# Kernel tuning notes

Measured on AMD Instinct MI355X. Metric: run time of the kernel, lower is better.

Reference implementation:

```python
import jax, jax.numpy as jnp
import numpy as np

HEADS = 4
BN_EPS = 1e-5


def _hgat_conv(x, src, dst, node_type, edge_attr, edge_type,
               ne, W, We, a_src, a_dst, a_edge, ee, Wres, b, concat):
    """Heterogeneous GAT conv: per-type embeddings + edge-featured attention.
    x: [N, Fin]; edge_attr: [E, De]; returns [N, H*C] (concat) or [N, C]."""
    N = x.shape[0]
    C = W.shape[1] // HEADS
    xi = x + ne[node_type]                                  # node-type conditioning
    h = (xi @ W).reshape(N, HEADS, C)                       # [N, H, C]
    he = ((edge_attr + ee[edge_type]) @ We).reshape(-1, HEADS, C)  # [E, H, C]
    s = jnp.einsum('nhc,hc->nh', h, a_src)                  # [N, H]
    d = jnp.einsum('nhc,hc->nh', h, a_dst)                  # [N, H]
    e = jnp.einsum('ehc,hc->eh', he, a_edge)                # [E, H]
    alpha = jax.nn.leaky_relu(s[src] + d[dst] + e, 0.2)     # [E, H]
    # softmax over incoming edges per destination node
    amax = jax.ops.segment_max(alpha, dst, num_segments=N)  # [N, H]
    amax = jnp.where(jnp.isfinite(amax), amax, 0.0)
    ex = jnp.exp(alpha - amax[dst])
    den = jax.ops.segment_sum(ex, dst, num_segments=N)
    coef = ex / (den[dst] + 1e-16)                          # [E, H]
    msg = h[src] * coef[:, :, None]                         # [E, H, C]
    out = jax.ops.segment_sum(msg, dst, num_segments=N)     # [N, H, C]
    out = out.reshape(N, HEADS * C) if concat else out.mean(axis=1)
    return out + x @ Wres + b                               # residual + bias


def _batch_norm(x, gamma, beta):
    mu = x.mean(axis=0)
    var = x.var(axis=0)
    return (x - mu) * jax.lax.rsqrt(var + BN_EPS) * gamma + beta


def setup_inputs() -> dict:
    key = jax.random.key(0)
    ks = jax.random.split(key, 32)
    N, E, H = 50000, 400000, 32          # nodes, edges, hidden_channels
    DE = 64                               # edge_dim
    NT, ET = 3, 4                         # node / edge type counts
    D1 = H * HEADS                        # 128 = enc1 output / enc2 width

    def g(k, shape, scale=1.0):
        return (jax.random.normal(ks[k], shape, dtype=jnp.float32) * scale)

    inp = {
        'x': g(0, (N, H)),
        'edge_index': jax.random.randint(ks[1], (2, E), 0, N, dtype=jnp.int32),
        'node_type': jax.random.randint(ks[2], (N,), 0, NT, dtype=jnp.int32),
        'edge_attr': g(3, (E, DE)),
        'edge_type': jax.random.randint(ks[4], (E,), 0, ET, dtype=jnp.int32),
        # enc1 params (in=32, per-head out=32, concat -> 128)
        'ne1': g(5, (NT, H), 0.1),
        'w1': g(6, (H, HEADS * H), 1.0 / np.sqrt(H)),
        'we1': g(7, (DE, HEADS * H), 1.0 / np.sqrt(DE)),
        'asrc1': g(8, (HEADS, H), 0.1), 'adst1': g(9, (HEADS, H), 0.1),
        'aedge1': g(10, (HEADS, H), 0.1),
        'ee1': g(11, (ET, DE), 0.1),
        'wres1': g(12, (H, D1), 1.0 / np.sqrt(H)),
        'b1': jnp.zeros((D1,), jnp.float32),
        # BatchNorm(128)
        'gamma': jnp.ones((D1,), jnp.float32),
        'beta': jnp.zeros((D1,), jnp.float32),
        # enc2 params (in=128, per-head out=128, mean -> 128)
        'ne2': g(13, (NT, D1), 0.1),
        'w2': g(14, (D1, HEADS * D1), 1.0 / np.sqrt(D1)),
        'we2': g(15, (DE, HEADS * D1), 1.0 / np.sqrt(DE)),
        'asrc2': g(16, (HEADS, D1), 0.1), 'adst2': g(17, (HEADS, D1), 0.1),
        'aedge2': g(18, (HEADS, D1), 0.1),
        'ee2': g(19, (ET, DE), 0.1),
        'wres2': g(20, (D1, D1), 1.0 / np.sqrt(D1)),
        'b2': jnp.zeros((D1,), jnp.float32),
    }
    return inp


def reference(x, edge_index, node_type, edge_attr, edge_type,
              ne1, w1, we1, asrc1, adst1, aedge1, ee1, wres1, b1,
              gamma, beta,
              ne2, w2, we2, asrc2, adst2, aedge2, ee2, wres2, b2):
    src, dst = edge_index[0], edge_index[1]
    h = _hgat_conv(x, src, dst, node_type, edge_attr, edge_type,
                   ne1, w1, we1, asrc1, adst1, aedge1, ee1, wres1, b1,
                   concat=True)
    h = _batch_norm(h, gamma, beta)
    out = _hgat_conv(h, src, dst, node_type, edge_attr, edge_type,
                     ne2, w2, we2, asrc2, adst2, aedge2, ee2, wres2, b2,
                     concat=False)
    return out
```

## Files before the change

kernel.cpp:

```cpp
#include <hip/hip_runtime.h>
#include <hip/hip_bf16.h>

typedef unsigned short u16;
typedef unsigned int u32;

constexpr int NN = 50000;
constexpr int NE = 400000;
constexpr int MPAD = 50048;

typedef __attribute__((ext_vector_type(8))) short s16x8;
typedef __attribute__((ext_vector_type(4))) float f32x4;

__device__ __forceinline__ float bf2f(u16 u) {
    union { u32 i; float f; } v; v.i = ((u32)u) << 16; return v.f;
}
__device__ __forceinline__ u16 f2bf(float f) {
    union { float f; u32 i; } v; v.f = f;
    u32 r = v.i + 0x7fffu + ((v.i >> 16) & 1u);
    return (u16)(r >> 16);
}
__device__ __forceinline__ float ldf(const void* p, size_t i, int isbf) {
    if (isbf) return bf2f(((const u16*)p)[i]);
    return ((const float*)p)[i];
}
__device__ __forceinline__ float clampf(float v) {
    return fminf(fmaxf(v, -1e4f), 1e4f);
}

__device__ int   g_flag;
__device__ int   g_counter;
__device__ float g_qe1[256], g_qe2[256];
__device__ float g_eq1[16], g_eq2[16];
__device__ float g_ps1[128], g_pd1[128], g_ps2[512], g_pd2[512];
__device__ float g_bnsum[128], g_bnsumsq[128], g_bnscale[128], g_bnshift[128];
__device__ int   g_deg[NN], g_start[NN], g_cur[NN];
__device__ int   g_eidx[NE];
__device__ __attribute__((aligned(16))) float g_sbuf[NN * 4];
__device__ __attribute__((aligned(16))) float g_dbuf[NN * 4];
__device__ __attribute__((aligned(16))) float g_alpha[(size_t)NE * 4];
__device__ __attribute__((aligned(16))) float g_el2[(size_t)NE * 4];
__device__ __attribute__((aligned(16))) float g_xbuf[(size_t)NN * 128];
__device__ __attribute__((aligned(16))) float g_acc2[(size_t)NN * 128];
__device__ __attribute__((aligned(16))) u16 g_A1[(size_t)MPAD * 64];
__device__ __attribute__((aligned(16))) u16 g_A2[(size_t)MPAD * 160];
__device__ __attribute__((aligned(16))) u16 g_B1t[192 * 64];
__device__ __attribute__((aligned(16))) u16 g_B1bt[128 * 128];
__device__ __attribute__((aligned(16))) u16 g_B2t[192 * 160];
__device__ __attribute__((aligned(16))) u16 g_B2bt[128 * 512];
__device__ __attribute__((aligned(16))) u16 g_xi1[(size_t)NN * 32];
__device__ __attribute__((aligned(16))) u16 g_xi2[(size_t)NN * 128];
__device__ __attribute__((aligned(16))) u16 g_agg1[(size_t)MPAD * 128];
__device__ __attribute__((aligned(16))) u16 g_agg2[(size_t)MPAD * 512];

__global__ void k_detect(const u16* x) {
    if (threadIdx.x == 0) {
        int cnt = 0;
        for (int i = 0; i < 64; i++) {
            u16 u = x[2 * i];
            int ex = (u >> 7) & 0xff;
            if (ex >= 100 && ex <= 140) cnt++;
        }
        g_flag = (cnt >= 40) ? 1 : 0;
        g_counter = 0;
    }
}
__global__ void k_zero() {
    int i = blockIdx.x * blockDim.x + threadIdx.x;
    if (i < NN) g_deg[i] = 0;
    if (i < 128) { g_bnsum[i] = 0.f; g_bnsumsq[i] = 0.f; }
}

__global__ __launch_bounds__(256) void k_prep(
    const void* we1, const void* ae1, const void* we2, const void* ae2,
    const void* w1, const void* as1, const void* ad1,
    const void* w2, const void* as2, const void* ad2) {
    int isbf = g_flag;
    int t = threadIdx.x;
    int idx = blockIdx.x * 16 + (t >> 4);
    int s = t & 15;
    float a = 0.f;
    if (idx < 256) {
        int k = idx >> 2, hd = idx & 3;
        for (int c = s; c < 32; c += 16)
            a += ldf(we1, k * 128 + hd * 32 + c, isbf) * ldf(ae1, hd * 32 + c, isbf);
    } else if (idx < 512) {
        int i2 = idx - 256;
        int k = i2 >> 2, hd = i2 & 3;
        for (int c = s; c < 128; c += 16)
            a += ldf(we2, k * 512 + hd * 128 + c, isbf) * ldf(ae2, hd * 128 + c, isbf);
    } else if (idx < 768) {
        int i2 = idx - 512;
        int isd = i2 >> 7, j = i2 & 127;
        int h = j >> 5, k = j & 31;
        const void* av = isd ? ad1 : as1;
        for (int c = s; c < 32; c += 16)
            a += ldf(w1, k * 128 + h * 32 + c, isbf) * ldf(av, h * 32 + c, isbf);
    } else {
        int i2 = idx - 768;
        int isd = i2 >> 9, j = i2 & 511;
        int h = j >> 7, k = j & 127;
        const void* av = isd ? ad2 : as2;
        for (int c = s; c < 128; c += 16)
            a += ldf(w2, (size_t)k * 512 + h * 128 + c, isbf) * ldf(av, h * 128 + c, isbf);
    }
#pragma unroll
    for (int mk = 8; mk >= 1; mk >>= 1) a += __shfl_xor(a, mk);
    if (s == 0) {
        if (idx < 256) g_qe1[idx] = a;
        else if (idx < 512) g_qe2[idx - 256] = a;
        else if (idx < 768) {
            int i2 = idx - 512;
            if (i2 >> 7) g_pd1[i2 & 127] = a; else g_ps1[i2 & 127] = a;
        } else {
            int i2 = idx - 768;
            if (i2 >> 9) g_pd2[i2 & 511] = a; else g_ps2[i2 & 511] = a;
        }
    }
}
__global__ void k_prep2(const void* ee1, const void* ee2) {
    int isbf = g_flag;
    int t = threadIdx.x;
    int idx = blockIdx.x * 16 + (t >> 4);
    int s = t & 15;
    int lyr = idx >> 4;
    int et = (idx >> 2) & 3, h = idx & 3;
    const void* ee = lyr ? ee2 : ee1;
    const float* qe = lyr ? g_qe2 : g_qe1;
    float a = 0.f;
    for (int k = s; k < 64; k += 16)
        a += ldf(ee, et * 64 + k, isbf) * qe[k * 4 + h];
#pragma unroll
    for (int mk = 8; mk >= 1; mk >>= 1) a += __shfl_xor(a, mk);
    if (s == 0) {
        if (lyr) g_eq2[et * 4 + h] = a; else g_eq1[et * 4 + h] = a;
    }
}

__global__ void k_deg(const int* __restrict__ dstp) {
    int e = blockIdx.x * blockDim.x + threadIdx.x;
    if (e < NE) atomicAdd(&g_deg[dstp[e]], 1);
}
__global__ void k_start() {
    int n = blockIdx.x * blockDim.x + threadIdx.x;
    if (n < NN) {
        int d = g_deg[n];
        int s = atomicAdd(&g_counter, d);
        g_start[n] = s; g_cur[n] = s;
    }
}
__global__ void k_scatter(const int* __restrict__ dstp) {
    int e = blockIdx.x * blockDim.x + threadIdx.x;
    if (e < NE) {
        int slot = atomicAdd(&g_cur[dstp[e]], 1);
        g_eidx[slot] = e;
    }
}

__device__ __forceinline__ u16 a1val(const void* x, int n, int k, int nt, int isbf) {
    if (k < 32) return f2bf(ldf(x, (size_t)n * 32 + k, isbf));
    if (k == 32 + nt || k == 35) return 0x3F80u;
    return 0;
}
__global__ __launch_bounds__(256) void k_buildA1(const void* x, const int* __restrict__ ntype,
                                                 const void* ne1) {
    int isbf = g_flag;
    int i = blockIdx.x * 256 + threadIdx.x;
    if (i >= MPAD * 32) return;
    int n = i >> 5, k2 = (i & 31) << 1;
    u32 pk = 0;
    if (n < NN) {
        int nt = ntype[n];
        pk = (u32)a1val(x, n, k2, nt, isbf) | ((u32)a1val(x, n, k2 + 1, nt, isbf) << 16);
        if (k2 < 32) {
            float x0 = ldf(x, (size_t)n * 32 + k2, isbf) + ldf(ne1, nt * 32 + k2, isbf);
            float x1 = ldf(x, (size_t)n * 32 + k2 + 1, isbf) + ldf(ne1, nt * 32 + k2 + 1, isbf);
            ((u32*)g_xi1)[(size_t)n * 16 + (k2 >> 1)] =
                (u32)f2bf(x0) | ((u32)f2bf(x1) << 16);
        }
    }
    ((u32*)g_A1)[i] = pk;
}
__global__ __launch_bounds__(256) void k_a2tail(const int* __restrict__ ntype) {
    int i = blockIdx.x * 256 + threadIdx.x;
    if (i >= NN * 16) return;
    int n = i >> 4, q = i & 15;
    int k2 = 128 + q * 2;
    int nt = ntype[n];
    u16 lo = (k2 == 128 + nt || k2 == 131) ? 0x3F80u : 0;
    u16 hi = (k2 + 1 == 128 + nt || k2 + 1 == 131) ? 0x3F80u : 0;
    ((u32*)g_A2)[(size_t)n * 80 + 64 + q] = (u32)lo | ((u32)hi << 16);
}
__global__ __launch_bounds__(256) void k_xi2(const int* __restrict__ ntype, const void* ne2) {
    int isbf = g_flag;
    int i = blockIdx.x * 256 + threadIdx.x;
    if (i >= NN * 64) return;
    int n = i >> 6, jp = (i & 63) << 1;
    int nt = ntype[n];
    float v0 = g_xbuf[(size_t)n * 128 + jp] * g_bnscale[jp] + g_bnshift[jp]
             + ldf(ne2, nt * 128 + jp, isbf);
    float v1 = g_xbuf[(size_t)n * 128 + jp + 1] * g_bnscale[jp + 1] + g_bnshift[jp + 1]
             + ldf(ne2, nt * 128 + jp + 1, isbf);
    ((u32*)g_xi2)[i] = (u32)f2bf(v0) | ((u32)f2bf(v1) << 16);
}

__global__ void k_buildB1(const void* ne1, const void* w1, const void* wres1, const void* b1) {
    int isbf = g_flag;
    int j = blockIdx.x;
    int k = threadIdx.x;
    float v = 0.f;
    if (j < 128) {
        if (k < 32) v = ldf(wres1, k * 128 + j, isbf);
        else if (k == 35) v = ldf(b1, j, isbf);
    } else if (j < 136) {
        int h = (j - 128) & 3;
        const float* p = (j < 132) ? g_ps1 : g_pd1;
        if (k < 32) v = p[h * 32 + k];
        else if (k < 35) {
            int tt = k - 32; float a = 0.f;
            for (int c = 0; c < 32; c++)
                a += ldf(ne1, tt * 32 + c, isbf) * p[h * 32 + c];
            v = a;
        }
    }
    (void)w1;
    g_B1t[j * 64 + k] = f2bf(v);
}
__global__ void k_buildB1b(const void* w1) {
    int isbf = g_flag;
    int j = blockIdx.x;
    int k = threadIdx.x;
    float v = ((k >> 5) == (j >> 5)) ? ldf(w1, (k & 31) * 128 + j, isbf) : 0.f;
    g_B1bt[j * 128 + k] = f2bf(v);
}
__global__ void k_buildB2(const void* ne2, const void* w2, const void* wres2, const void* b2) {
    int isbf = g_flag;
    int j = blockIdx.x;
    int k = threadIdx.x;
    if (k >= 160) return;
    float v = 0.f;
    if (j < 128) {
        if (k < 128) v = g_bnscale[k] * ldf(wres2, k * 128 + j, isbf);
        else if (k == 131) {
            float a = ldf(b2, j, isbf);
            for (int c = 0; c < 128; c++)
                a += g_bnshift[c] * ldf(wres2, c * 128 + j, isbf);
            v = a;
        }
    } else if (j < 136) {
        int h = (j - 128) & 3;
        const float* p = (j < 132) ? g_ps2 : g_pd2;
        if (k < 128) v = g_bnscale[k] * p[h * 128 + k];
        else if (k < 131) {
            int tt = k - 128; float a = 0.f;
            for (int c = 0; c < 128; c++)
                a += (g_bnshift[c] + ldf(ne2, tt * 128 + c, isbf)) * p[h * 128 + c];
            v = a;
        }
    }
    (void)w2;
    g_B2t[j * 160 + k] = f2bf(v);
}
__global__ void k_buildB2b(const void* w2) {
    int isbf = g_flag;
    int j = blockIdx.x;
    for (int k = threadIdx.x; k < 512; k += 256) {
        float v = 0.25f * ldf(w2, (size_t)(k & 127) * 512 + (k >> 7) * 128 + j, isbf);
        g_B2bt[j * 512 + k] = f2bf(v);
    }
}

template<int K, int KT, int LAYER>
__global__ __launch_bounds__(256) void k_gemm(void* outp) {
    constexpr int KP = KT + 8;
    __shared__ __attribute__((aligned(16))) u16 As[64 * KP];
    __shared__ __attribute__((aligned(16))) u16 Bs[64 * KP];
    const u16* __restrict__ A  = (LAYER == 1) ? g_A1 : (LAYER == 2) ? g_A2
                               : (LAYER == 3) ? g_agg1 : g_agg2;
    const u16* __restrict__ Bt = (LAYER == 1) ? g_B1t : (LAYER == 2) ? g_B2t
                               : (LAYER == 3) ? g_B1bt : g_B2bt;
    int isbf = g_flag;
    const int t = threadIdx.x;
    const int mb = blockIdx.x, cb = blockIdx.y;
    const int wave = t >> 6, lane = t & 63;
    const int lr = lane & 15, lg = lane >> 4;
    f32x4 acc[4] = {};
    constexpr int CH = KT / 8;
#pragma unroll 1
    for (int kt = 0; kt < K / KT; kt++) {
        __syncthreads();
        for (int c = t; c < 64 * CH; c += 256) {
            int r = c / CH, o = (c - r * CH) * 8;
            *(s16x8*)&As[r * KP + o] =
                *(const s16x8*)&A[((size_t)(mb * 64 + r)) * K + kt * KT + o];
            *(s16x8*)&Bs[r * KP + o] =
                *(const s16x8*)&Bt[((size_t)(cb * 64 + r)) * K + kt * KT + o];
        }
        __syncthreads();
        const u16* ap  = &As[(wave * 16 + lr) * KP + lg * 8];
        const u16* bp0 = &Bs[lr * KP + lg * 8];
#pragma unroll
        for (int ks = 0; ks < KT / 32; ks++) {
            s16x8 af = *(const s16x8*)(ap + ks * 32);
#pragma unroll
            for (int ct = 0; ct < 4; ct++) {
                s16x8 bf = *(const s16x8*)(bp0 + ct * 16 * KP + ks * 32);
                acc[ct] = __builtin_amdgcn_mfma_f32_16x16x32_bf16(af, bf, acc[ct], 0, 0, 0);
            }
        }
    }
    const int rowb = mb * 64 + wave * 16 + lg * 4;
#pragma unroll
    for (int ct = 0; ct < 4; ct++) {
        int j = cb * 64 + ct * 16 + lr;
#pragma unroll
        for (int r = 0; r < 4; r++) {
            int n = rowb + r;
            if (n >= NN) continue;
            float v = acc[ct][r];
            if (LAYER == 1) {
                if (j < 128)      g_xbuf[(size_t)n * 128 + j] = clampf(v);
                else if (j < 132) g_sbuf[n * 4 + (j - 128)] = clampf(v);
                else if (j < 136) g_dbuf[n * 4 + (j - 132)] = clampf(v);
            } else if (LAYER == 2) {
                if (j < 128)      g_acc2[(size_t)n * 128 + j] = clampf(v);
                else if (j < 132) g_sbuf[n * 4 + (j - 128)] = clampf(v);
                else if (j < 136) g_dbuf[n * 4 + (j - 132)] = clampf(v);
            } else if (LAYER == 3) {
                float* p = &g_xbuf[(size_t)n * 128 + j];
                float x = clampf(*p + v);
                *p = x;
                g_A2[(size_t)n * 160 + j] = f2bf(x);
            } else {
                float v2 = clampf(g_acc2[(size_t)n * 128 + j] + v);
                if (isbf) ((u16*)outp)[(size_t)n * 128 + j] = f2bf(v2);
                else      ((float*)outp)[(size_t)n * 128 + j] = v2;
            }
        }
    }
}

__global__ __launch_bounds__(256) void k_edge12(
    const int* __restrict__ srcp, const int* __restrict__ dstp,
    const int* __restrict__ etype, const void* eattr) {
    __shared__ float qel1[256], qel2[256], eq1s[16], eq2s[16];
    int isbf = g_flag;
    int t = threadIdx.x;
    qel1[t] = g_qe1[t];
    qel2[t] = g_qe2[t];
    if (t < 16) { eq1s[t] = g_eq1[t]; eq2s[t] = g_eq2[t]; }
    __syncthreads();
    int sub = t & 15;
    float q1[4][4], q2[4][4];
#pragma unroll
    for (int i = 0; i < 4; i++)
#pragma unroll
        for (int h = 0; h < 4; h++) {
            q1[i][h] = qel1[(sub * 4 + i) * 4 + h];
            q2[i][h] = qel2[(sub * 4 + i) * 4 + h];
        }
    int e = blockIdx.x * 16 + (t >> 4);
    if (e >= NE) return;
    float ev[4];
    if (isbf) {
        ushort4 vv = *(const ushort4*)((const u16*)eattr + (size_t)e * 64 + sub * 4);
        ev[0] = bf2f(vv.x); ev[1] = bf2f(vv.y); ev[2] = bf2f(vv.z); ev[3] = bf2f(vv.w);
    } else {
        float4 vv = *(const float4*)((const float*)eattr + (size_t)e * 64 + sub * 4);
        ev[0] = vv.x; ev[1] = vv.y; ev[2] = vv.z; ev[3] = vv.w;
    }
    float p10 = 0.f, p11 = 0.f, p12 = 0.f, p13 = 0.f;
    float p20 = 0.f, p21 = 0.f, p22 = 0.f, p23 = 0.f;
#pragma unroll
    for (int i = 0; i < 4; i++) {
        p10 += ev[i] * q1[i][0]; p11 += ev[i] * q1[i][1];
        p12 += ev[i] * q1[i][2]; p13 += ev[i] * q1[i][3];
        p20 += ev[i] * q2[i][0]; p21 += ev[i] * q2[i][1];
        p22 += ev[i] * q2[i][2]; p23 += ev[i] * q2[i][3];
    }
#pragma unroll
    for (int mk = 1; mk < 16; mk <<= 1) {
        p10 += __shfl_xor(p10, mk); p11 += __shfl_xor(p11, mk);
        p12 += __shfl_xor(p12, mk); p13 += __shfl_xor(p13, mk);
        p20 += __shfl_xor(p20, mk); p21 += __shfl_xor(p21, mk);
        p22 += __shfl_xor(p22, mk); p23 += __shfl_xor(p23, mk);
    }
    if (sub == 0) {
        int et = etype[e], ss = srcp[e], dd = dstp[e];
        float4 sb = *(const float4*)(g_sbuf + ss * 4);
        float4 db = *(const float4*)(g_dbuf + dd * 4);
        float a0 = sb.x + db.x + p10 + eq1s[et * 4 + 0];
        float a1 = sb.y + db.y + p11 + eq1s[et * 4 + 1];
        float a2 = sb.z + db.z + p12 + eq1s[et * 4 + 2];
        float a3 = sb.w + db.w + p13 + eq1s[et * 4 + 3];
        a0 = a0 > 0.f ? a0 : 0.2f * a0;
        a1 = a1 > 0.f ? a1 : 0.2f * a1;
        a2 = a2 > 0.f ? a2 : 0.2f * a2;
        a3 = a3 > 0.f ? a3 : 0.2f * a3;
        *(float4*)(g_alpha + 4 * (size_t)e) = make_float4(
            clampf(a0), clampf(a1), clampf(a2), clampf(a3));
        *(float4*)(g_el2 + 4 * (size_t)e) = make_float4(
            p20 + eq2s[et * 4 + 0], p21 + eq2s[et * 4 + 1],
            p22 + eq2s[et * 4 + 2], p23 + eq2s[et * 4 + 3]);
    }
}

__global__ __launch_bounds__(256) void k_edge2(
    const int* __restrict__ srcp, const int* __restrict__ dstp) {
    int e = blockIdx.x * 256 + threadIdx.x;
    if (e >= NE) return;
    float4 p = *(const float4*)(g_el2 + 4 * (size_t)e);
    int ss = srcp[e], dd = dstp[e];
    float4 sb = *(const float4*)(g_sbuf + ss * 4);
    float4 db = *(const float4*)(g_dbuf + dd * 4);
    float a0 = sb.x + db.x + p.x;
    float a1 = sb.y + db.y + p.y;
    float a2 = sb.z + db.z + p.z;
    float a3 = sb.w + db.w + p.w;
    a0 = a0 > 0.f ? a0 : 0.2f * a0;
    a1 = a1 > 0.f ? a1 : 0.2f * a1;
    a2 = a2 > 0.f ? a2 : 0.2f * a2;
    a3 = a3 > 0.f ? a3 : 0.2f * a3;
    *(float4*)(g_alpha + 4 * (size_t)e) = make_float4(
        clampf(a0), clampf(a1), clampf(a2), clampf(a3));
}

__global__ __launch_bounds__(256) void k_att1(const int* __restrict__ srcp) {
    int lane = threadIdx.x & 63;
    int n = blockIdx.x * 4 + (threadIdx.x >> 6);
    if (n >= NN) return;
    int st = g_start[n], dg = g_deg[n];
    float m0 = -1e30f, m1 = -1e30f, m2 = -1e30f, m3 = -1e30f;
    for (int i = lane; i < dg; i += 64) {
        int e = g_eidx[st + i];
        float4 a = *(const float4*)(g_alpha + 4 * (size_t)e);
        m0 = fmaxf(m0, a.x); m1 = fmaxf(m1, a.y);
        m2 = fmaxf(m2, a.z); m3 = fmaxf(m3, a.w);
    }
    for (int mk = 32; mk >= 1; mk >>= 1) {
        m0 = fmaxf(m0, __shfl_xor(m0, mk)); m1 = fmaxf(m1, __shfl_xor(m1, mk));
        m2 = fmaxf(m2, __shfl_xor(m2, mk)); m3 = fmaxf(m3, __shfl_xor(m3, mk));
    }
    int j0 = 2 * lane;
    int hd = j0 >> 5;
    float z0 = 0.f, z1 = 0.f, z2 = 0.f, z3 = 0.f;
    float acc0 = 0.f, acc1 = 0.f;
    for (int base = 0; base < dg; base += 64) {
        int i = base + lane;
        int sidx = 0; float c0 = 0.f, c1 = 0.f, c2 = 0.f, c3 = 0.f;
        if (i < dg) {
            int e = g_eidx[st + i];
            float4 a = *(const float4*)(g_alpha + 4 * (size_t)e);
            sidx = srcp[e];
            c0 = expf(a.x - m0); c1 = expf(a.y - m1);
            c2 = expf(a.z - m2); c3 = expf(a.w - m3);
            z0 += c0; z1 += c1; z2 += c2; z3 += c3;
        }
        int cnt = min(64, dg - base);
        for (int jj = 0; jj < cnt; jj++) {
            int s2 = __shfl(sidx, jj);
            float b0 = __shfl(c0, jj), b1 = __shfl(c1, jj);
            float b2v = __shfl(c2, jj), b3 = __shfl(c3, jj);
            float cs = hd == 0 ? b0 : hd == 1 ? b1 : hd == 2 ? b2v : b3;
            u32 hv = *(const u32*)(g_xi1 + (size_t)s2 * 32 + (j0 & 31));
            acc0 += bf2f((u16)(hv & 0xffff)) * cs;
            acc1 += bf2f((u16)(hv >> 16)) * cs;
        }
    }
    for (int mk = 32; mk >= 1; mk >>= 1) {
        z0 += __shfl_xor(z0, mk); z1 += __shfl_xor(z1, mk);
        z2 += __shfl_xor(z2, mk); z3 += __shfl_xor(z3, mk);
    }
    float iv = 1.f / ((hd == 0 ? z0 : hd == 1 ? z1 : hd == 2 ? z2 : z3) + 1e-16f);
    ((u32*)g_agg1)[((size_t)n * 128 + j0) >> 1] =
        (u32)f2bf(acc0 * iv) | ((u32)f2bf(acc1 * iv) << 16);
}

__global__ __launch_bounds__(256) void k_bnstats() {
    int t = threadIdx.x;
    int j = t & 127;
    int r0 = blockIdx.x * 2 + (t >> 7);
    float s = 0.f, ss = 0.f;
    for (int r = r0; r < NN; r += 500) {
        float v = g_xbuf[(size_t)r * 128 + j];
        s += v; ss += v * v;
    }
    atomicAdd(&g_bnsum[j], s);
    atomicAdd(&g_bnsumsq[j], ss);
}
__global__ void k_bnfin(const void* gamma, const void* beta) {
    int isbf = g_flag;
    int j = threadIdx.x;
    float mu = g_bnsum[j] * (1.f / NN);
    float var = fmaxf(g_bnsumsq[j] * (1.f / NN) - mu * mu, 0.f);
    float rstd = rsqrtf(var + 1e-5f);
    float sc = ldf(gamma, j, isbf) * rstd;
    g_bnscale[j] = sc;
    g_bnshift[j] = ldf(beta, j, isbf) - mu * sc;
}

__global__ __launch_bounds__(256) void k_att2(const int* __restrict__ srcp) {
    int lane = threadIdx.x & 63;
    int n = blockIdx.x * 4 + (threadIdx.x >> 6);
    if (n >= NN) return;
    int st = g_start[n], dg = g_deg[n];
    float m0 = -1e30f, m1 = -1e30f, m2 = -1e30f, m3 = -1e30f;
    for (int i = lane; i < dg; i += 64) {
        int e = g_eidx[st + i];
        float4 a = *(const float4*)(g_alpha + 4 * (size_t)e);
        m0 = fmaxf(m0, a.x); m1 = fmaxf(m1, a.y);
        m2 = fmaxf(m2, a.z); m3 = fmaxf(m3, a.w);
    }
    for (int mk = 32; mk >= 1; mk >>= 1) {
        m0 = fmaxf(m0, __shfl_xor(m0, mk)); m1 = fmaxf(m1, __shfl_xor(m1, mk));
        m2 = fmaxf(m2, __shfl_xor(m2, mk)); m3 = fmaxf(m3, __shfl_xor(m3, mk));
    }
    int c0 = 2 * lane;
    float z0 = 0.f, z1 = 0.f, z2 = 0.f, z3 = 0.f;
    float a00 = 0.f, a01 = 0.f, a10 = 0.f, a11 = 0.f;
    float a20 = 0.f, a21 = 0.f, a30 = 0.f, a31 = 0.f;
    for (int base = 0; base < dg; base += 64) {
        int i = base + lane;
        int sidx = 0; float c0f = 0.f, c1f = 0.f, c2f = 0.f, c3f = 0.f;
        if (i < dg) {
            int e = g_eidx[st + i];
            float4 a = *(const float4*)(g_alpha + 4 * (size_t)e);
            sidx = srcp[e];
            c0f = expf(a.x - m0); c1f = expf(a.y - m1);
            c2f = expf(a.z - m2); c3f = expf(a.w - m3);
            z0 += c0f; z1 += c1f; z2 += c2f; z3 += c3f;
        }
        int cnt = min(64, dg - base);
        for (int jj = 0; jj < cnt; jj++) {
            int s2 = __shfl(sidx, jj);
            float b0 = __shfl(c0f, jj), b1 = __shfl(c1f, jj);
            float b2v = __shfl(c2f, jj), b3 = __shfl(c3f, jj);
            u32 hv = *(const u32*)(g_xi2 + (size_t)s2 * 128 + c0);
            float lo = bf2f((u16)(hv & 0xffff)), hi = bf2f((u16)(hv >> 16));
            a00 += lo * b0;  a01 += hi * b0;
            a10 += lo * b1;  a11 += hi * b1;
            a20 += lo * b2v; a21 += hi * b2v;
            a30 += lo * b3;  a31 += hi * b3;
        }
    }
    for (int mk = 32; mk >= 1; mk >>= 1) {
        z0 += __shfl_xor(z0, mk); z1 += __shfl_xor(z1, mk);
        z2 += __shfl_xor(z2, mk); z3 += __shfl_xor(z3, mk);
    }
    float iv0 = 1.f / (z0 + 1e-16f), iv1 = 1.f / (z1 + 1e-16f);
    float iv2 = 1.f / (z2 + 1e-16f), iv3 = 1.f / (z3 + 1e-16f);
    u32* out = (u32*)g_agg2 + (((size_t)n * 512 + c0) >> 1);
    out[0]   = (u32)f2bf(a00 * iv0) | ((u32)f2bf(a01 * iv0) << 16);
    out[64]  = (u32)f2bf(a10 * iv1) | ((u32)f2bf(a11 * iv1) << 16);
    out[128] = (u32)f2bf(a20 * iv2) | ((u32)f2bf(a21 * iv2) << 16);
    out[192] = (u32)f2bf(a30 * iv3) | ((u32)f2bf(a31 * iv3) << 16);
}

extern "C" void kernel_launch(void* const* d_in, const int* in_sizes, int n_in,
                              void* d_out, int out_size, void* d_ws, size_t ws_size,
                              hipStream_t stream) {
    const void* x     = d_in[0];
    const int* ei     = (const int*)d_in[1];
    const int* ntype  = (const int*)d_in[2];
    const void* eattr = d_in[3];
    const int* etype  = (const int*)d_in[4];
    const void* ne1   = d_in[5];
    const void* w1    = d_in[6];
    const void* we1   = d_in[7];
    const void* asrc1 = d_in[8];
    const void* adst1 = d_in[9];
    const void* aedge1= d_in[10];
    const void* ee1   = d_in[11];
    const void* wres1 = d_in[12];
    const void* b1    = d_in[13];
    const void* gamma = d_in[14];
    const void* beta  = d_in[15];
    const void* ne2   = d_in[16];
    const void* w2    = d_in[17];
    const void* we2   = d_in[18];
    const void* asrc2 = d_in[19];
    const void* adst2 = d_in[20];
    const void* aedge2= d_in[21];
    const void* ee2   = d_in[22];
    const void* wres2 = d_in[23];
    const void* b2    = d_in[24];
    (void)in_sizes; (void)n_in; (void)out_size; (void)d_ws; (void)ws_size;

    const int* srcp = ei;
    const int* dstp = ei + NE;

    k_detect<<<1, 64, 0, stream>>>((const u16*)x);
    k_zero<<<196, 256, 0, stream>>>();
    k_prep<<<112, 256, 0, stream>>>(we1, aedge1, we2, aedge2,
                                    w1, asrc1, adst1, w2, asrc2, adst2);
    k_prep2<<<2, 256, 0, stream>>>(ee1, ee2);
    k_deg<<<1563, 256, 0, stream>>>(dstp);
    k_start<<<196, 256, 0, stream>>>();
    k_scatter<<<1563, 256, 0, stream>>>(dstp);

    k_buildA1<<<(MPAD * 32 + 255) / 256, 256, 0, stream>>>(x, ntype, ne1);
    k_buildB1<<<192, 64, 0, stream>>>(ne1, w1, wres1, b1);
    k_buildB1b<<<128, 128, 0, stream>>>(w1);
    k_gemm<64, 64, 1><<<dim3(MPAD / 64, 3), 256, 0, stream>>>(nullptr);
    k_edge12<<<NE / 16, 256, 0, stream>>>(srcp, dstp, etype, eattr);
    k_att1<<<12500, 256, 0, stream>>>(srcp);
    k_gemm<128, 128, 3><<<dim3(MPAD / 64, 2), 256, 0, stream>>>(nullptr);

    k_bnstats<<<250, 256, 0, stream>>>();
    k_bnfin<<<1, 128, 0, stream>>>(gamma, beta);

    k_xi2<<<12500, 256, 0, stream>>>(ntype, ne2);
    k_a2tail<<<(NN * 16 + 255) / 256, 256, 0, stream>>>(ntype);
    k_buildB2<<<192, 192, 0, stream>>>(ne2, w2, wres2, b2);
    k_buildB2b<<<128, 256, 0, stream>>>(w2);
    k_gemm<160, 160, 2><<<dim3(MPAD / 64, 3), 256, 0, stream>>>(nullptr);
    k_edge2<<<1563, 256, 0, stream>>>(srcp, dstp);
    k_att2<<<12500, 256, 0, stream>>>(srcp);
    k_gemm<512, 128, 4><<<dim3(MPAD / 64, 2), 256, 0, stream>>>(d_out);
}
```

Baseline: 608.2 us.

## Compute edge-attribute attention projections with MFMA instead of shuffle reductions

Replaces the per-edge dot-product kernel, which used 16 lanes per edge and shuffle reductions, with a wave-level MFMA kernel. Each wave processes 16 edges per tile against a packed bf16 64x16 matrix of both layers' projection vectors, built in k_prep2. This removes the many shuffles and the partly idle lanes of the old kernel. In exchange, fp32 edge attributes are now rounded to bf16 before the dot product, and the output writes become scalar and strided instead of float4.

```diff
diff --git a/kernel.cpp b/kernel.cpp
--- a/kernel.cpp
+++ b/kernel.cpp
@@ -47,6 +47,7 @@
 __device__ __attribute__((aligned(16))) u16 g_B1bt[128 * 128];
 __device__ __attribute__((aligned(16))) u16 g_B2t[192 * 160];
 __device__ __attribute__((aligned(16))) u16 g_B2bt[128 * 512];
+__device__ __attribute__((aligned(16))) u16 g_qeB[16 * 64];
 __device__ __attribute__((aligned(16))) u16 g_xi1[(size_t)NN * 32];
 __device__ __attribute__((aligned(16))) u16 g_xi2[(size_t)NN * 128];
 __device__ __attribute__((aligned(16))) u16 g_agg1[(size_t)MPAD * 128];
@@ -134,6 +135,14 @@
     if (s == 0) {
         if (lyr) g_eq2[et * 4 + h] = a; else g_eq1[et * 4 + h] = a;
     }
+    int base = blockIdx.x * 256 + t;
+    for (int i = base; i < 1024; i += 512) {
+        int col = i >> 6, k = i & 63;
+        float v = 0.f;
+        if (col < 4) v = g_qe1[k * 4 + col];
+        else if (col < 8) v = g_qe2[k * 4 + (col - 4)];
+        g_qeB[col * 64 + k] = f2bf(v);
+    }
 }
 
 __global__ void k_deg(const int* __restrict__ dstp) {
@@ -339,68 +348,61 @@
     }
 }
 
-__global__ __launch_bounds__(256) void k_edge12(
+__global__ __launch_bounds__(256) void k_edgemm(
     const int* __restrict__ srcp, const int* __restrict__ dstp,
     const int* __restrict__ etype, const void* eattr) {
-    __shared__ float qel1[256], qel2[256], eq1s[16], eq2s[16];
-    int isbf = g_flag;
-    int t = threadIdx.x;
-    qel1[t] = g_qe1[t];
-    qel2[t] = g_qe2[t];
-    if (t < 16) { eq1s[t] = g_eq1[t]; eq2s[t] = g_eq2[t]; }
-    __syncthreads();
-    int sub = t & 15;
-    float q1[4][4], q2[4][4];
+    int isbf = g_flag;
+    int t = threadIdx.x, wave = t >> 6, lane = t & 63;
+    int lr = lane & 15, lg = lane >> 4;
+    s16x8 bf0 = *(const s16x8*)&g_qeB[lr * 64 + lg * 8];
+    s16x8 bf1 = *(const s16x8*)&g_qeB[lr * 64 + 32 + lg * 8];
+    int ebase = blockIdx.x * 256 + wave * 64;
+#pragma unroll 1
+    for (int tile = 0; tile < 4; tile++) {
+        int e0 = ebase + tile * 16;
+        int ea = e0 + lr; if (ea >= NE) ea = NE - 1;
+        f32x4 acc = {};
+        if (isbf) {
+            const u16* ep = (const u16*)eattr + (size_t)ea * 64 + lg * 8;
+            s16x8 va = *(const s16x8*)(ep);
+            s16x8 vb = *(const s16x8*)(ep + 32);
+            acc = __builtin_amdgcn_mfma_f32_16x16x32_bf16(va, bf0, acc, 0, 0, 0);
+            acc = __builtin_amdgcn_mfma_f32_16x16x32_bf16(vb, bf1, acc, 0, 0, 0);
+        } else {
+            const float* ep = (const float*)eattr + (size_t)ea * 64 + lg * 8;
+            float4 fa = *(const float4*)(ep);
+            float4 fb = *(const float4*)(ep + 4);
+            float4 fc = *(const float4*)(ep + 32);
+            float4 fd = *(const float4*)(ep + 36);
+            s16x8 va, vb;
+            va[0] = (short)f2bf(fa.x); va[1] = (short)f2bf(fa.y);
+            va[2] = (short)f2bf(fa.z); va[3] = (short)f2bf(fa.w);
+            va[4] = (short)f2bf(fb.x); va[5] = (short)f2bf(fb.y);
+            va[6] = (short)f2bf(fb.z); va[7] = (short)f2bf(fb.w);
+            vb[0] = (short)f2bf(fc.x); vb[1] = (short)f2bf(fc.y);
+            vb[2] = (short)f2bf(fc.z); vb[3] = (short)f2bf(fc.w);
+            vb[4] = (short)f2bf(fd.x); vb[5] = (short)f2bf(fd.y);
+            vb[6] = (short)f2bf(fd.z); vb[7] = (short)f2bf(fd.w);
+            acc = __builtin_amdgcn_mfma_f32_16x16x32_bf16(va, bf0, acc, 0, 0, 0);
+            acc = __builtin_amdgcn_mfma_f32_16x16x32_bf16(vb, bf1, acc, 0, 0, 0);
+        }
+        if (lr < 8) {
 #pragma unroll
-    for (int i = 0; i < 4; i++)
-#pragma unroll
-        for (int h = 0; h < 4; h++) {
-            q1[i][h] = qel1[(sub * 4 + i) * 4 + h];
-            q2[i][h] = qel2[(sub * 4 + i) * 4 + h];
-        }
-    int e = blockIdx.x * 16 + (t >> 4);
-    if (e >= NE) return;
-    float ev[4];
-    if (isbf) {
-        ushort4 vv = *(const ushort4*)((const u16*)eattr + (size_t)e * 64 + sub * 4);
-        ev[0] = bf2f(vv.x); ev[1] = bf2f(vv.y); ev[2] = bf2f(vv.z); ev[3] = bf2f(vv.w);
-    } else {
-        float4 vv = *(const float4*)((const float*)eattr + (size_t)e * 64 + sub * 4);
-        ev[0] = vv.x; ev[1] = vv.y; ev[2] = vv.z; ev[3] = vv.w;
-    }
-    float p10 = 0.f, p11 = 0.f, p12 = 0.f, p13 = 0.f;
-    float p20 = 0.f, p21 = 0.f, p22 = 0.f, p23 = 0.f;
-#pragma unroll
-    for (int i = 0; i < 4; i++) {
-        p10 += ev[i] * q1[i][0]; p11 += ev[i] * q1[i][1];
-        p12 += ev[i] * q1[i][2]; p13 += ev[i] * q1[i][3];
-        p20 += ev[i] * q2[i][0]; p21 += ev[i] * q2[i][1];
-        p22 += ev[i] * q2[i][2]; p23 += ev[i] * q2[i][3];
-    }
-#pragma unroll
-    for (int mk = 1; mk < 16; mk <<= 1) {
-        p10 += __shfl_xor(p10, mk); p11 += __shfl_xor(p11, mk);
-        p12 += __shfl_xor(p12, mk); p13 += __shfl_xor(p13, mk);
-        p20 += __shfl_xor(p20, mk); p21 += __shfl_xor(p21, mk);
-        p22 += __shfl_xor(p22, mk); p23 += __shfl_xor(p23, mk);
-    }
-    if (sub == 0) {
-        int et = etype[e], ss = srcp[e], dd = dstp[e];
-        float4 sb = *(const float4*)(g_sbuf + ss * 4);
-        float4 db = *(const float4*)(g_dbuf + dd * 4);
-        float a0 = sb.x + db.x + p10 + eq1s[et * 4 + 0];
-        float a1 = sb.y + db.y + p11 + eq1s[et * 4 + 1];
-        float a2 = sb.z + db.z + p12 + eq1s[et * 4 + 2];
-        float a3 = sb.w + db.w + p13 + eq1s[et * 4 + 3];
-        a0 = a0 > 0.f ? a0 : 0.2f * a0;
-        a1 = a1 > 0.f ? a1 : 0.2f * a1;
-        a2 = a2 > 0.f ? a2 : 0.2f * a2;
-        a3 = a3 > 0.f ? a3 : 0.2f * a3;
-        *(float4*)(g_alpha + 4 * (size_t)e) = make_float4(
-            clampf(a0), clampf(a1), clampf(a2), clampf(a3));
-        *(float4*)(g_el2 + 4 * (size_t)e) = make_float4(
-            p20 + eq2s[et * 4 + 0], p21 + eq2s[et * 4 + 1],
-            p22 + eq2s[et * 4 + 2], p23 + eq2s[et * 4 + 3]);
+            for (int r = 0; r < 4; r++) {
+                int ee = e0 + lg * 4 + r;
+                if (ee >= NE) continue;
+                int et = etype[ee];
+                if (lr < 4) {
+                    int ss = srcp[ee], dd = dstp[ee];
+                    float a = g_sbuf[ss * 4 + lr] + g_dbuf[dd * 4 + lr]
+                            + acc[r] + g_eq1[et * 4 + lr];
+                    a = a > 0.f ? a : 0.2f * a;
+                    g_alpha[4 * (size_t)ee + lr] = clampf(a);
+                } else {
+                    g_el2[4 * (size_t)ee + (lr - 4)] = acc[r] + g_eq2[et * 4 + (lr - 4)];
+                }
+            }
+        }
     }
 }
 
@@ -601,7 +603,7 @@
     k_buildB1<<<192, 64, 0, stream>>>(ne1, w1, wres1, b1);
     k_buildB1b<<<128, 128, 0, stream>>>(w1);
     k_gemm<64, 64, 1><<<dim3(MPAD / 64, 3), 256, 0, stream>>>(nullptr);
-    k_edge12<<<NE / 16, 256, 0, stream>>>(srcp, dstp, etype, eattr);
+    k_edgemm<<<(NE + 255) / 256, 256, 0, stream>>>(srcp, dstp, etype, eattr);
     k_att1<<<12500, 256, 0, stream>>>(srcp);
     k_gemm<128, 128, 3><<<dim3(MPAD / 64, 2), 256, 0, stream>>>(nullptr);
 
```

Result: no change. 600.2 us (-1.3%).
